# Optimization experiments

Hardware: AMD Instinct MI355X
Metric: run time of the kernel (lower is better)

The kernel has to match this reference:

```python
import jax, jax.numpy as jnp
import numpy as np

P = 0.8  # DropConnect keep probability
KERNELS = (3, 2)


def eps_contract(core, x, ks):
    """Contract one EPS core with all sliding ks x ks windows of x.
    core: (out, q**(ks*ks)); x: (b, h, w, q) -> (b, h-ks+1, w-ks+1, out).
    Builds the window tensor-product incrementally (small fixed ks*ks loop)."""
    b, h, w, q = x.shape
    H, W = h - ks + 1, w - ks + 1
    prod = None
    for di in range(ks):
        for dj in range(ks):
            pix = x[:, di:di + H, dj:dj + W, :]  # (b, H, W, q)
            if prod is None:
                prod = pix
            else:
                prod = (prod[..., :, None] * pix[..., None, :]).reshape(b, H, W, -1)
    # prod: (b, H, W, q**(ks*ks))
    return jnp.einsum('bhwk,ok->bhwo', prod, core)


def dropconnect_epses(epses):
    """Bernoulli(P) mask each core's components, rescale by 1/P (training mode)."""
    mkey = jax.random.key(42)
    out = []
    for i, core in enumerate(epses):
        mask = (jax.random.uniform(jax.random.fold_in(mkey, i), core.shape) < P).astype(core.dtype)
        out.append(mask * core / P)
    return out


def setup_inputs() -> dict:
    key = jax.random.key(0)
    k0, k1, k2, k3 = jax.random.split(key, 4)
    b = 128
    x = jax.random.uniform(k0, (b, 28, 28, 2), jnp.float32)  # quantum-encoded image
    d0 = 2 ** (3 * 3)   # 512 : first core input dim (q=2, ks=3)
    d1 = 6 ** (2 * 2)   # 1296: second core input dim (q=6, ks=2)
    eps0 = jax.random.normal(k1, (6, d0), jnp.float32) * d0 ** -0.5
    eps1 = jax.random.normal(k2, (10, d1), jnp.float32) * d1 ** -0.5
    in_features = 25 * 25 * 10  # (28 - (3+2) + 2)^2 * out_q
    W = jax.random.normal(k3, (10, in_features), jnp.float32) * (in_features ** -0.5 / 4.0)
    bias = jnp.zeros((10,), jnp.float32)
    return {"x": x, "eps0": eps0, "eps1": eps1, "W": W, "bias": bias}


def reference(x, eps0, eps1, W, bias):
    e0, e1 = dropconnect_epses((eps0, eps1))
    h = eps_contract(e0, x, KERNELS[0])   # (b, 26, 26, 6)
    h = eps_contract(e1, h, KERNELS[1])   # (b, 25, 25, 10)
    flat = h.reshape(h.shape[0], -1)      # b (h w q)
    return flat @ W.T + bias
```

## Files before the change

### kernel.cpp

```cpp
#include <hip/hip_runtime.h>
#include <hip/hip_bf16.h>
#include <stdint.h>

typedef __attribute__((ext_vector_type(8))) short short8;
typedef __attribute__((ext_vector_type(4))) float floatx4;
typedef __attribute__((ext_vector_type(4))) int intx4;

__device__ __forceinline__ void threefry2x32(uint32_t k0, uint32_t k1,
                                             uint32_t& x0, uint32_t& x1) {
  const uint32_t ks2 = k0 ^ k1 ^ 0x1BD11BDAu;
  uint32_t ks[3] = {k0, k1, ks2};
  const int rot[8] = {13, 15, 26, 6, 17, 29, 16, 24};
  x0 += ks[0];
  x1 += ks[1];
#pragma unroll
  for (int i = 0; i < 5; ++i) {
#pragma unroll
    for (int j = 0; j < 4; ++j) {
      const int r = rot[(i & 1) * 4 + j];
      x0 += x1;
      x1 = (x1 << r) | (x1 >> (32 - r));
      x1 ^= x0;
    }
    x0 += ks[(i + 1) % 3];
    x1 += ks[(i + 2) % 3] + (uint32_t)(i + 1);
  }
}

__device__ __forceinline__ float dropmask(int core, int e, float v) {
  uint32_t f0 = 0u, f1 = (uint32_t)core;
  threefry2x32(0u, 42u, f0, f1);
  uint32_t a = 0u, b = (uint32_t)e;
  threefry2x32(f0, f1, a, b);
  uint32_t bits = a ^ b;
  float u = __uint_as_float((bits >> 9) | 0x3F800000u) - 1.0f;
  float m = (u < 0.8f) ? 1.0f : 0.0f;
  return v * m / 0.8f;
}

__device__ __forceinline__ unsigned short f2bf(float f) {
  uint32_t u = __float_as_uint(f);
  uint32_t r = u + 0x7fffu + ((u >> 16) & 1u);
  return (unsigned short)(r >> 16);
}

union B2I { __hip_bfloat162 b; int i; };
__device__ __forceinline__ int pk_bf16(float lo, float hi) {
  B2I u;
  u.b = __float22bfloat162_rn(make_float2(lo, hi));
  return u.i;
}
union Frag { intx4 i; short8 s; };

__global__ void prep_kernel(const float* __restrict__ eps0,
                            const float* __restrict__ eps1,
                            unsigned short* __restrict__ bsw1,
                            unsigned short* __restrict__ bsw2,
                            float* __restrict__ out) {
  int idx = blockIdx.x * 256 + threadIdx.x;
  if (idx < 1280) out[idx] = 0.0f;
  if (idx < 8192) {
    int j = idx & 7, L = (idx >> 3) & 63, c = idx >> 9;
    int o = L & 15, q = L >> 4;
    int k = c * 32 + q * 8 + j;
    float v = 0.0f;
    if (o < 6) {
      int e = o * 512 + k;
      v = dropmask(0, e, eps0[e]);
    }
    bsw1[idx] = f2bf(v);
  } else {
    int t2 = idx - 8192;
    int j = t2 & 7, L = (t2 >> 3) & 63, c = t2 >> 9;
    int o = L & 15, q = L >> 4;
    int t = 45 * q + c;
    int m = t / 5, nk = 8 * (t % 5) + j;
    float v = 0.0f;
    if (o < 10 && nk < 36) {
      int e = o * 1296 + m * 36 + nk;
      v = dropmask(1, e, eps1[e]);
    }
    bsw2[t2] = f2bf(v);
  }
}

__device__ __forceinline__ float sel6(const float a[6], int k) {
  float r = a[0];
  r = (k == 1) ? a[1] : r;
  r = (k == 2) ? a[2] : r;
  r = (k == 3) ? a[3] : r;
  r = (k == 4) ? a[4] : r;
  r = (k == 5) ? a[5] : r;
  return r;
}

__global__ __launch_bounds__(256, 2) void stage1_mfma(
    const float* __restrict__ x, const unsigned short* __restrict__ bsw1,
    float* __restrict__ h) {
  __shared__ intx4 Bs[1024];
  {
    const intx4* src = (const intx4*)bsw1;
#pragma unroll
    for (int t = 0; t < 4; ++t)
      Bs[threadIdx.x + 256 * t] = src[threadIdx.x + 256 * t];
  }
  __syncthreads();

  const int lane = threadIdx.x & 63;
  const int wave = (blockIdx.x * 256 + threadIdx.x) >> 6;
  const int col = lane & 15, q = lane >> 4;
  const int pid = wave * 16 + col;
  const int b = pid / 676;
  const int rem = pid - b * 676;
  const int ii = rem / 26;
  const int jj = rem - ii * 26;

  const float2* x2 = (const float2*)x;
  float xv[9][2];
#pragma unroll
  for (int di = 0; di < 3; ++di)
#pragma unroll
    for (int dj = 0; dj < 3; ++dj) {
      float2 v = x2[(b * 28 + ii + di) * 28 + (jj + dj)];
      xv[di * 3 + dj][0] = v.x;
      xv[di * 3 + dj][1] = v.y;
    }

  float w3[8];
#pragma unroll
  for (int j = 0; j < 8; ++j)
    w3[j] = xv[6][(j >> 2) & 1] * xv[7][(j >> 1) & 1] * xv[8][j & 1];

  const float wq = xv[4][(q >> 1) & 1] * xv[5][q & 1];
  float t01[4], t23[4];
#pragma unroll
  for (int a = 0; a < 2; ++a)
#pragma unroll
    for (int d = 0; d < 2; ++d) {
      t01[a * 2 + d] = xv[0][a] * xv[1][d];
      t23[a * 2 + d] = xv[2][a] * xv[3][d] * wq;
    }

  floatx4 acc0 = {0.f, 0.f, 0.f, 0.f};
  floatx4 acc1 = {0.f, 0.f, 0.f, 0.f};
#pragma unroll
  for (int c = 0; c < 16; ++c) {
    Frag bf;
    bf.i = Bs[c * 64 + lane];
    const float w = t01[c >> 2] * t23[c & 3];
    float av[8];
#pragma unroll
    for (int j = 0; j < 8; ++j) av[j] = w * w3[j];
    Frag af;
    af.i.x = pk_bf16(av[0], av[1]);
    af.i.y = pk_bf16(av[2], av[3]);
    af.i.z = pk_bf16(av[4], av[5]);
    af.i.w = pk_bf16(av[6], av[7]);
    if (c & 1)
      acc1 = __builtin_amdgcn_mfma_f32_16x16x32_bf16(af.s, bf.s, acc1, 0, 0, 0);
    else
      acc0 = __builtin_amdgcn_mfma_f32_16x16x32_bf16(af.s, bf.s, acc0, 0, 0, 0);
  }
  const floatx4 acc = acc0 + acc1;
  if (col < 6) {
#pragma unroll
    for (int r = 0; r < 4; ++r) h[(wave * 16 + q * 4 + r) * 6 + col] = acc[r];
  }
}

__global__ __launch_bounds__(256, 2) void stage2_mfma(
    const float* __restrict__ h, const unsigned short* __restrict__ bsw2,
    float* __restrict__ flat) {
  __shared__ intx4 Bs[2880];
  {
    const intx4* src = (const intx4*)bsw2;
    for (int t = threadIdx.x; t < 2880; t += 256) Bs[t] = src[t];
  }
  __syncthreads();

  const int lane = threadIdx.x & 63;
  const int wave = (blockIdx.x * 256 + threadIdx.x) >> 6;
  const int col = lane & 15, q = lane >> 4;
  const int pid = wave * 16 + col;
  const int b = pid / 625;
  const int rem = pid - b * 625;
  const int ii = rem / 25;
  const int jj = rem - ii * 25;

  const float* hp = h + ((b * 26 + ii) * 26 + jj) * 6;
  float h00[6], h01[6], h10[6], h11[6];
  const float2* hp2a = (const float2*)(hp);
  const float2* hp2b = (const float2*)(hp + 156);
#pragma unroll
  for (int t = 0; t < 3; ++t) {
    float2 v0 = hp2a[t], v1 = hp2a[t + 3], v2 = hp2b[t], v3 = hp2b[t + 3];
    h00[2 * t] = v0.x; h00[2 * t + 1] = v0.y;
    h01[2 * t] = v1.x; h01[2 * t + 1] = v1.y;
    h10[2 * t] = v2.x; h10[2 * t + 1] = v2.y;
    h11[2 * t] = v3.x; h11[2 * t + 1] = v3.y;
  }

  floatx4 acc0 = {0.f, 0.f, 0.f, 0.f};
  floatx4 acc1 = {0.f, 0.f, 0.f, 0.f};
#pragma unroll
  for (int d = 0; d < 9; ++d) {
    const int m = 9 * q + d;
    const int ia = (m * 43) >> 8;
    const int ic = m - ia * 6;
    const float p01 = sel6(h00, ia) * sel6(h01, ic);
    float ph[6];
#pragma unroll
    for (int a = 0; a < 6; ++a) ph[a] = p01 * h10[a];
#pragma unroll
    for (int e = 0; e < 5; ++e) {
      Frag bf;
      bf.i = Bs[(d * 5 + e) * 64 + lane];
      const int n0 = 8 * e;
      float av[8];
#pragma unroll
      for (int j = 0; j < 8; ++j) {
        const int n = n0 + j;
        av[j] = (n < 36) ? ph[n / 6] * h11[n % 6] : 0.0f;
      }
      Frag af;
      af.i.x = pk_bf16(av[0], av[1]);
      af.i.y = pk_bf16(av[2], av[3]);
      af.i.z = pk_bf16(av[4], av[5]);
      af.i.w = pk_bf16(av[6], av[7]);
      if (e & 1)
        acc1 = __builtin_amdgcn_mfma_f32_16x16x32_bf16(af.s, bf.s, acc1, 0, 0, 0);
      else
        acc0 = __builtin_amdgcn_mfma_f32_16x16x32_bf16(af.s, bf.s, acc0, 0, 0, 0);
    }
  }
  const floatx4 acc = acc0 + acc1;
  if (col < 10) {
#pragma unroll
    for (int r = 0; r < 4; ++r)
      flat[(wave * 16 + q * 4 + r) * 10 + col] = acc[r];
  }
}

__global__ __launch_bounds__(256) void linear_kernel(
    const float* __restrict__ flat, const float* __restrict__ W,
    const float* __restrict__ bias, float* __restrict__ out) {
  const int b = blockIdx.x;
  const int c = blockIdx.y;
  const float* fb = flat + b * 6250 + c * 1250;
  const float* Wc = W + c * 1250;
  float acc[10];
#pragma unroll
  for (int o = 0; o < 10; ++o) acc[o] = 0.0f;
  for (int f = threadIdx.x; f < 1250; f += 256) {
    const float v = fb[f];
#pragma unroll
    for (int o = 0; o < 10; ++o) acc[o] += v * Wc[o * 6250 + f];
  }
#pragma unroll
  for (int o = 0; o < 10; ++o) {
#pragma unroll
    for (int s = 32; s > 0; s >>= 1) acc[o] += __shfl_xor(acc[o], s, 64);
  }
  __shared__ float red[4][10];
  const int lane = threadIdx.x & 63, wv = threadIdx.x >> 6;
  if (lane == 0) {
#pragma unroll
    for (int o = 0; o < 10; ++o) red[wv][o] = acc[o];
  }
  __syncthreads();
  if (threadIdx.x < 10) {
    const int o = threadIdx.x;
    float r = red[0][o] + red[1][o] + red[2][o] + red[3][o];
    if (c == 0) r += bias[o];
    atomicAdd(&out[b * 10 + o], r);
  }
}

extern "C" void kernel_launch(void* const* d_in, const int* in_sizes, int n_in,
                              void* d_out, int out_size, void* d_ws,
                              size_t ws_size, hipStream_t stream) {
  const float* x = (const float*)d_in[0];
  const float* eps0 = (const float*)d_in[1];
  const float* eps1 = (const float*)d_in[2];
  const float* W = (const float*)d_in[3];
  const float* bias = (const float*)d_in[4];
  float* out = (float*)d_out;

  char* wsb = (char*)d_ws;
  unsigned short* bsw1 = (unsigned short*)wsb;
  unsigned short* bsw2 = (unsigned short*)(wsb + 16384);
  float* h = (float*)(wsb + 65536);
  float* flat = (float*)(wsb + 65536 + 2076672);

  hipLaunchKernelGGL(prep_kernel, dim3(122), dim3(256), 0, stream, eps0, eps1,
                     bsw1, bsw2, out);
  hipLaunchKernelGGL(stage1_mfma, dim3(1352), dim3(256), 0, stream, x, bsw1,
                     h);
  hipLaunchKernelGGL(stage2_mfma, dim3(1250), dim3(256), 0, stream, h, bsw2,
                     flat);
  hipLaunchKernelGGL(linear_kernel, dim3(128, 5), dim3(256), 0, stream, flat,
                     W, bias, out);
}
```

Measured before the change: 105.1 us.

## Fuse both EPS stages and linear layer into one per-batch kernel

Merges stage1, stage2 and the linear layer into a single kernel with one 512-thread block per batch element. The intermediates h and flat stay in shared memory instead of global memory, and the B fragments are held in registers rather than LDS. The output is written directly, which removes the atomics and the zeroing in the prep kernel. The cost is that only 128 blocks run, which may underfill the GPU's CUs, and the 45 intx4 register fragments raise register pressure.

```diff
diff --git a/kernel.cpp b/kernel.cpp
--- a/kernel.cpp
+++ b/kernel.cpp
@@ -55,10 +55,8 @@
 __global__ void prep_kernel(const float* __restrict__ eps0,
                             const float* __restrict__ eps1,
                             unsigned short* __restrict__ bsw1,
-                            unsigned short* __restrict__ bsw2,
-                            float* __restrict__ out) {
+                            unsigned short* __restrict__ bsw2) {
   int idx = blockIdx.x * 256 + threadIdx.x;
-  if (idx < 1280) out[idx] = 0.0f;
   if (idx < 8192) {
     int j = idx & 7, L = (idx >> 3) & 63, c = idx >> 9;
     int o = L & 15, q = L >> 4;
@@ -94,185 +92,174 @@
   return r;
 }
 
-__global__ __launch_bounds__(256, 2) void stage1_mfma(
+__global__ __launch_bounds__(512, 2) void fused_kernel(
     const float* __restrict__ x, const unsigned short* __restrict__ bsw1,
-    float* __restrict__ h) {
-  __shared__ intx4 Bs[1024];
-  {
-    const intx4* src = (const intx4*)bsw1;
-#pragma unroll
-    for (int t = 0; t < 4; ++t)
-      Bs[threadIdx.x + 256 * t] = src[threadIdx.x + 256 * t];
-  }
-  __syncthreads();
-
-  const int lane = threadIdx.x & 63;
-  const int wave = (blockIdx.x * 256 + threadIdx.x) >> 6;
+    const unsigned short* __restrict__ bsw2, const float* __restrict__ W,
+    const float* __restrict__ bias, float* __restrict__ out) {
+  __shared__ float h_lds[4056];
+  __shared__ float flat_lds[6250];
+  __shared__ float red[8][10];
+
+  const int b = blockIdx.x;
+  const int tid = threadIdx.x;
+  const int lane = tid & 63;
+  const int wv = tid >> 6;
   const int col = lane & 15, q = lane >> 4;
-  const int pid = wave * 16 + col;
-  const int b = pid / 676;
-  const int rem = pid - b * 676;
-  const int ii = rem / 26;
-  const int jj = rem - ii * 26;
-
-  const float2* x2 = (const float2*)x;
-  float xv[9][2];
-#pragma unroll
-  for (int di = 0; di < 3; ++di)
-#pragma unroll
-    for (int dj = 0; dj < 3; ++dj) {
-      float2 v = x2[(b * 28 + ii + di) * 28 + (jj + dj)];
-      xv[di * 3 + dj][0] = v.x;
-      xv[di * 3 + dj][1] = v.y;
-    }
-
-  float w3[8];
-#pragma unroll
-  for (int j = 0; j < 8; ++j)
-    w3[j] = xv[6][(j >> 2) & 1] * xv[7][(j >> 1) & 1] * xv[8][j & 1];
-
-  const float wq = xv[4][(q >> 1) & 1] * xv[5][q & 1];
-  float t01[4], t23[4];
-#pragma unroll
-  for (int a = 0; a < 2; ++a)
-#pragma unroll
-    for (int d = 0; d < 2; ++d) {
-      t01[a * 2 + d] = xv[0][a] * xv[1][d];
-      t23[a * 2 + d] = xv[2][a] * xv[3][d] * wq;
-    }
-
-  floatx4 acc0 = {0.f, 0.f, 0.f, 0.f};
-  floatx4 acc1 = {0.f, 0.f, 0.f, 0.f};
-#pragma unroll
-  for (int c = 0; c < 16; ++c) {
-    Frag bf;
-    bf.i = Bs[c * 64 + lane];
-    const float w = t01[c >> 2] * t23[c & 3];
-    float av[8];
-#pragma unroll
-    for (int j = 0; j < 8; ++j) av[j] = w * w3[j];
-    Frag af;
-    af.i.x = pk_bf16(av[0], av[1]);
-    af.i.y = pk_bf16(av[2], av[3]);
-    af.i.z = pk_bf16(av[4], av[5]);
-    af.i.w = pk_bf16(av[6], av[7]);
-    if (c & 1)
-      acc1 = __builtin_amdgcn_mfma_f32_16x16x32_bf16(af.s, bf.s, acc1, 0, 0, 0);
-    else
-      acc0 = __builtin_amdgcn_mfma_f32_16x16x32_bf16(af.s, bf.s, acc0, 0, 0, 0);
-  }
-  const floatx4 acc = acc0 + acc1;
-  if (col < 6) {
-#pragma unroll
-    for (int r = 0; r < 4; ++r) h[(wave * 16 + q * 4 + r) * 6 + col] = acc[r];
-  }
-}
-
-__global__ __launch_bounds__(256, 2) void stage2_mfma(
-    const float* __restrict__ h, const unsigned short* __restrict__ bsw2,
-    float* __restrict__ flat) {
-  __shared__ intx4 Bs[2880];
-  {
-    const intx4* src = (const intx4*)bsw2;
-    for (int t = threadIdx.x; t < 2880; t += 256) Bs[t] = src[t];
-  }
-  __syncthreads();
-
-  const int lane = threadIdx.x & 63;
-  const int wave = (blockIdx.x * 256 + threadIdx.x) >> 6;
-  const int col = lane & 15, q = lane >> 4;
-  const int pid = wave * 16 + col;
-  const int b = pid / 625;
-  const int rem = pid - b * 625;
-  const int ii = rem / 25;
-  const int jj = rem - ii * 25;
-
-  const float* hp = h + ((b * 26 + ii) * 26 + jj) * 6;
-  float h00[6], h01[6], h10[6], h11[6];
-  const float2* hp2a = (const float2*)(hp);
-  const float2* hp2b = (const float2*)(hp + 156);
-#pragma unroll
-  for (int t = 0; t < 3; ++t) {
-    float2 v0 = hp2a[t], v1 = hp2a[t + 3], v2 = hp2b[t], v3 = hp2b[t + 3];
-    h00[2 * t] = v0.x; h00[2 * t + 1] = v0.y;
-    h01[2 * t] = v1.x; h01[2 * t + 1] = v1.y;
-    h10[2 * t] = v2.x; h10[2 * t + 1] = v2.y;
-    h11[2 * t] = v3.x; h11[2 * t + 1] = v3.y;
-  }
-
-  floatx4 acc0 = {0.f, 0.f, 0.f, 0.f};
-  floatx4 acc1 = {0.f, 0.f, 0.f, 0.f};
-#pragma unroll
-  for (int d = 0; d < 9; ++d) {
-    const int m = 9 * q + d;
-    const int ia = (m * 43) >> 8;
-    const int ic = m - ia * 6;
-    const float p01 = sel6(h00, ia) * sel6(h01, ic);
-    float ph[6];
-#pragma unroll
-    for (int a = 0; a < 6; ++a) ph[a] = p01 * h10[a];
-#pragma unroll
-    for (int e = 0; e < 5; ++e) {
+
+  intx4 bfr1[16];
+  const intx4* bsrc1 = (const intx4*)bsw1;
+#pragma unroll
+  for (int c = 0; c < 16; ++c) bfr1[c] = bsrc1[c * 64 + lane];
+
+  const float2* x2 = (const float2*)x + b * 784;
+#pragma unroll 1
+  for (int tile = wv; tile < 43; tile += 8) {
+    const int p_raw = tile * 16 + col;
+    const int p = p_raw < 676 ? p_raw : 675;
+    const int ii = p / 26, jj = p - (p / 26) * 26;
+
+    float xv[9][2];
+#pragma unroll
+    for (int di = 0; di < 3; ++di)
+#pragma unroll
+      for (int dj = 0; dj < 3; ++dj) {
+        float2 v = x2[(ii + di) * 28 + (jj + dj)];
+        xv[di * 3 + dj][0] = v.x;
+        xv[di * 3 + dj][1] = v.y;
+      }
+
+    float w3[8];
+#pragma unroll
+    for (int j = 0; j < 8; ++j)
+      w3[j] = xv[6][(j >> 2) & 1] * xv[7][(j >> 1) & 1] * xv[8][j & 1];
+
+    const float wq = xv[4][(q >> 1) & 1] * xv[5][q & 1];
+    float t01[4], t23[4];
+#pragma unroll
+    for (int a = 0; a < 2; ++a)
+#pragma unroll
+      for (int d = 0; d < 2; ++d) {
+        t01[a * 2 + d] = xv[0][a] * xv[1][d];
+        t23[a * 2 + d] = xv[2][a] * xv[3][d] * wq;
+      }
+
+    floatx4 acc0 = {0.f, 0.f, 0.f, 0.f};
+    floatx4 acc1 = {0.f, 0.f, 0.f, 0.f};
+#pragma unroll
+    for (int c = 0; c < 16; ++c) {
       Frag bf;
-      bf.i = Bs[(d * 5 + e) * 64 + lane];
-      const int n0 = 8 * e;
-      float av[8];
-#pragma unroll
-      for (int j = 0; j < 8; ++j) {
-        const int n = n0 + j;
-        av[j] = (n < 36) ? ph[n / 6] * h11[n % 6] : 0.0f;
-      }
+      bf.i = bfr1[c];
+      const float w = t01[c >> 2] * t23[c & 3];
       Frag af;
-      af.i.x = pk_bf16(av[0], av[1]);
-      af.i.y = pk_bf16(av[2], av[3]);
-      af.i.z = pk_bf16(av[4], av[5]);
-      af.i.w = pk_bf16(av[6], av[7]);
-      if (e & 1)
+      af.i.x = pk_bf16(w * w3[0], w * w3[1]);
+      af.i.y = pk_bf16(w * w3[2], w * w3[3]);
+      af.i.z = pk_bf16(w * w3[4], w * w3[5]);
+      af.i.w = pk_bf16(w * w3[6], w * w3[7]);
+      if (c & 1)
         acc1 = __builtin_amdgcn_mfma_f32_16x16x32_bf16(af.s, bf.s, acc1, 0, 0, 0);
       else
         acc0 = __builtin_amdgcn_mfma_f32_16x16x32_bf16(af.s, bf.s, acc0, 0, 0, 0);
     }
-  }
-  const floatx4 acc = acc0 + acc1;
-  if (col < 10) {
-#pragma unroll
-    for (int r = 0; r < 4; ++r)
-      flat[(wave * 16 + q * 4 + r) * 10 + col] = acc[r];
-  }
-}
-
-__global__ __launch_bounds__(256) void linear_kernel(
-    const float* __restrict__ flat, const float* __restrict__ W,
-    const float* __restrict__ bias, float* __restrict__ out) {
-  const int b = blockIdx.x;
-  const int c = blockIdx.y;
-  const float* fb = flat + b * 6250 + c * 1250;
-  const float* Wc = W + c * 1250;
+    const floatx4 acc = acc0 + acc1;
+    if (col < 6) {
+#pragma unroll
+      for (int r = 0; r < 4; ++r) {
+        const int pp = tile * 16 + q * 4 + r;
+        if (pp < 676) h_lds[pp * 6 + col] = acc[r];
+      }
+    }
+  }
+
+  intx4 bfr2[45];
+  const intx4* bsrc2 = (const intx4*)bsw2;
+#pragma unroll
+  for (int c = 0; c < 45; ++c) bfr2[c] = bsrc2[c * 64 + lane];
+
+  __syncthreads();
+
+#pragma unroll 1
+  for (int tile = wv; tile < 40; tile += 8) {
+    const int p_raw = tile * 16 + col;
+    const int p = p_raw < 625 ? p_raw : 624;
+    const int ii = p / 25, jj = p - (p / 25) * 25;
+    const int hbase = (ii * 26 + jj) * 6;
+
+    float h00[6], h01[6], h10[6], h11[6];
+#pragma unroll
+    for (int t = 0; t < 6; ++t) {
+      h00[t] = h_lds[hbase + t];
+      h01[t] = h_lds[hbase + 6 + t];
+      h10[t] = h_lds[hbase + 156 + t];
+      h11[t] = h_lds[hbase + 162 + t];
+    }
+
+    floatx4 acc0 = {0.f, 0.f, 0.f, 0.f};
+    floatx4 acc1 = {0.f, 0.f, 0.f, 0.f};
+#pragma unroll
+    for (int d = 0; d < 9; ++d) {
+      const int m = 9 * q + d;
+      const int ia = (m * 43) >> 8;
+      const int ic = m - ia * 6;
+      const float p01 = sel6(h00, ia) * sel6(h01, ic);
+      float ph[6];
+#pragma unroll
+      for (int a = 0; a < 6; ++a) ph[a] = p01 * h10[a];
+#pragma unroll
+      for (int e = 0; e < 5; ++e) {
+        Frag bf;
+        bf.i = bfr2[d * 5 + e];
+        const int n0 = 8 * e;
+        float av[8];
+#pragma unroll
+        for (int j = 0; j < 8; ++j) {
+          const int n = n0 + j;
+          av[j] = (n < 36) ? ph[n / 6] * h11[n % 6] : 0.0f;
+        }
+        Frag af;
+        af.i.x = pk_bf16(av[0], av[1]);
+        af.i.y = pk_bf16(av[2], av[3]);
+        af.i.z = pk_bf16(av[4], av[5]);
+        af.i.w = pk_bf16(av[6], av[7]);
+        if (e & 1)
+          acc1 = __builtin_amdgcn_mfma_f32_16x16x32_bf16(af.s, bf.s, acc1, 0, 0, 0);
+        else
+          acc0 = __builtin_amdgcn_mfma_f32_16x16x32_bf16(af.s, bf.s, acc0, 0, 0, 0);
+      }
+    }
+    const floatx4 acc = acc0 + acc1;
+    if (col < 10) {
+#pragma unroll
+      for (int r = 0; r < 4; ++r) {
+        const int pp = tile * 16 + q * 4 + r;
+        if (pp < 625) flat_lds[pp * 10 + col] = acc[r];
+      }
+    }
+  }
+  __syncthreads();
+
   float acc[10];
 #pragma unroll
   for (int o = 0; o < 10; ++o) acc[o] = 0.0f;
-  for (int f = threadIdx.x; f < 1250; f += 256) {
-    const float v = fb[f];
-#pragma unroll
-    for (int o = 0; o < 10; ++o) acc[o] += v * Wc[o * 6250 + f];
+  for (int f = tid; f < 6250; f += 512) {
+    const float v = flat_lds[f];
+#pragma unroll
+    for (int o = 0; o < 10; ++o) acc[o] += v * W[o * 6250 + f];
   }
 #pragma unroll
   for (int o = 0; o < 10; ++o) {
 #pragma unroll
     for (int s = 32; s > 0; s >>= 1) acc[o] += __shfl_xor(acc[o], s, 64);
   }
-  __shared__ float red[4][10];
-  const int lane = threadIdx.x & 63, wv = threadIdx.x >> 6;
   if (lane == 0) {
 #pragma unroll
     for (int o = 0; o < 10; ++o) red[wv][o] = acc[o];
   }
   __syncthreads();
-  if (threadIdx.x < 10) {
-    const int o = threadIdx.x;
-    float r = red[0][o] + red[1][o] + red[2][o] + red[3][o];
-    if (c == 0) r += bias[o];
-    atomicAdd(&out[b * 10 + o], r);
+  if (tid < 10) {
+    float r = bias[tid];
+#pragma unroll
+    for (int ww = 0; ww < 8; ++ww) r += red[ww][tid];
+    out[b * 10 + tid] = r;
   }
 }
 
@@ -289,15 +276,9 @@
   char* wsb = (char*)d_ws;
   unsigned short* bsw1 = (unsigned short*)wsb;
   unsigned short* bsw2 = (unsigned short*)(wsb + 16384);
-  float* h = (float*)(wsb + 65536);
-  float* flat = (float*)(wsb + 65536 + 2076672);
 
   hipLaunchKernelGGL(prep_kernel, dim3(122), dim3(256), 0, stream, eps0, eps1,
-                     bsw1, bsw2, out);
-  hipLaunchKernelGGL(stage1_mfma, dim3(1352), dim3(256), 0, stream, x, bsw1,
-                     h);
-  hipLaunchKernelGGL(stage2_mfma, dim3(1250), dim3(256), 0, stream, h, bsw2,
-                     flat);
-  hipLaunchKernelGGL(linear_kernel, dim3(128, 5), dim3(256), 0, stream, flat,
-                     W, bias, out);
-}
+                     bsw1, bsw2);
+  hipLaunchKernelGGL(fused_kernel, dim3(128), dim3(512), 0, stream, x, bsw1,
+                     bsw2, W, bias, out);
+}
```

Result: no change. 103.8 us (-1.2%).

## Switch MFMA stages to fp16 with packed half2 products and register-held B fragments

Applied to the files above, without the earlier changes.

Switches both contraction stages from bf16 to fp16 MFMA. The A-fragment outer products are now built with packed half2 multiplies instead of fp32 multiplies followed by bf16 packing. The shared-memory staging of the masked cores and its block barrier are replaced by per-lane global loads into registers, with an 8-deep prefetch ring in stage 2, and the launch-bounds occupancy hint rises from 2 to 4. Doing the products in half precision cuts conversion ALU work but changes rounding and narrows range, and the register-held fragments raise register pressure.

```diff
diff --git a/kernel.cpp b/kernel.cpp
--- a/kernel.cpp
+++ b/kernel.cpp
@@ -1,8 +1,8 @@
 #include <hip/hip_runtime.h>
-#include <hip/hip_bf16.h>
 #include <stdint.h>
 
-typedef __attribute__((ext_vector_type(8))) short short8;
+typedef _Float16 half8 __attribute__((ext_vector_type(8)));
+typedef _Float16 half2v __attribute__((ext_vector_type(2)));
 typedef __attribute__((ext_vector_type(4))) float floatx4;
 typedef __attribute__((ext_vector_type(4))) int intx4;
 
@@ -38,19 +38,14 @@
   return v * m / 0.8f;
 }
 
-__device__ __forceinline__ unsigned short f2bf(float f) {
-  uint32_t u = __float_as_uint(f);
-  uint32_t r = u + 0x7fffu + ((u >> 16) & 1u);
-  return (unsigned short)(r >> 16);
-}
-
-union B2I { __hip_bfloat162 b; int i; };
-__device__ __forceinline__ int pk_bf16(float lo, float hi) {
-  B2I u;
-  u.b = __float22bfloat162_rn(make_float2(lo, hi));
-  return u.i;
-}
-union Frag { intx4 i; short8 s; };
+union H2U { _Float16 h; unsigned short s; };
+__device__ __forceinline__ unsigned short f2h(float f) {
+  H2U u;
+  u.h = (_Float16)f;
+  return u.s;
+}
+
+union FragH { intx4 i; half8 h; half2v h2[4]; };
 
 __global__ void prep_kernel(const float* __restrict__ eps0,
                             const float* __restrict__ eps1,
@@ -68,7 +63,7 @@
       int e = o * 512 + k;
       v = dropmask(0, e, eps0[e]);
     }
-    bsw1[idx] = f2bf(v);
+    bsw1[idx] = f2h(v);
   } else {
     int t2 = idx - 8192;
     int j = t2 & 7, L = (t2 >> 3) & 63, c = t2 >> 9;
@@ -80,7 +75,7 @@
       int e = o * 1296 + m * 36 + nk;
       v = dropmask(1, e, eps1[e]);
     }
-    bsw2[t2] = f2bf(v);
+    bsw2[t2] = f2h(v);
   }
 }
 
@@ -94,21 +89,18 @@
   return r;
 }
 
-__global__ __launch_bounds__(256, 2) void stage1_mfma(
+__global__ __launch_bounds__(256, 4) void stage1_mfma(
     const float* __restrict__ x, const unsigned short* __restrict__ bsw1,
     float* __restrict__ h) {
-  __shared__ intx4 Bs[1024];
-  {
-    const intx4* src = (const intx4*)bsw1;
-#pragma unroll
-    for (int t = 0; t < 4; ++t)
-      Bs[threadIdx.x + 256 * t] = src[threadIdx.x + 256 * t];
-  }
-  __syncthreads();
-
   const int lane = threadIdx.x & 63;
   const int wave = (blockIdx.x * 256 + threadIdx.x) >> 6;
   const int col = lane & 15, q = lane >> 4;
+
+  intx4 bfr1[16];
+  const intx4* bsrc1 = (const intx4*)bsw1 + lane;
+#pragma unroll
+  for (int c = 0; c < 16; ++c) bfr1[c] = bsrc1[c * 64];
+
   const int pid = wave * 16 + col;
   const int b = pid / 676;
   const int rem = pid - b * 676;
@@ -126,10 +118,14 @@
       xv[di * 3 + dj][1] = v.y;
     }
 
-  float w3[8];
-#pragma unroll
-  for (int j = 0; j < 8; ++j)
-    w3[j] = xv[6][(j >> 2) & 1] * xv[7][(j >> 1) & 1] * xv[8][j & 1];
+  half2v w3p[4];
+#pragma unroll
+  for (int p2 = 0; p2 < 4; ++p2) {
+    const int j0 = 2 * p2, j1 = j0 + 1;
+    const float a0 = xv[6][(j0 >> 2) & 1] * xv[7][(j0 >> 1) & 1] * xv[8][j0 & 1];
+    const float a1 = xv[6][(j1 >> 2) & 1] * xv[7][(j1 >> 1) & 1] * xv[8][j1 & 1];
+    w3p[p2] = half2v{(_Float16)a0, (_Float16)a1};
+  }
 
   const float wq = xv[4][(q >> 1) & 1] * xv[5][q & 1];
   float t01[4], t23[4];
@@ -145,21 +141,19 @@
   floatx4 acc1 = {0.f, 0.f, 0.f, 0.f};
 #pragma unroll
   for (int c = 0; c < 16; ++c) {
-    Frag bf;
-    bf.i = Bs[c * 64 + lane];
-    const float w = t01[c >> 2] * t23[c & 3];
-    float av[8];
-#pragma unroll
-    for (int j = 0; j < 8; ++j) av[j] = w * w3[j];
-    Frag af;
-    af.i.x = pk_bf16(av[0], av[1]);
-    af.i.y = pk_bf16(av[2], av[3]);
-    af.i.z = pk_bf16(av[4], av[5]);
-    af.i.w = pk_bf16(av[6], av[7]);
+    FragH bf;
+    bf.i = bfr1[c];
+    const _Float16 wh = (_Float16)(t01[c >> 2] * t23[c & 3]);
+    const half2v w2 = {wh, wh};
+    FragH af;
+    af.h2[0] = w2 * w3p[0];
+    af.h2[1] = w2 * w3p[1];
+    af.h2[2] = w2 * w3p[2];
+    af.h2[3] = w2 * w3p[3];
     if (c & 1)
-      acc1 = __builtin_amdgcn_mfma_f32_16x16x32_bf16(af.s, bf.s, acc1, 0, 0, 0);
+      acc1 = __builtin_amdgcn_mfma_f32_16x16x32_f16(af.h, bf.h, acc1, 0, 0, 0);
     else
-      acc0 = __builtin_amdgcn_mfma_f32_16x16x32_bf16(af.s, bf.s, acc0, 0, 0, 0);
+      acc0 = __builtin_amdgcn_mfma_f32_16x16x32_f16(af.h, bf.h, acc0, 0, 0, 0);
   }
   const floatx4 acc = acc0 + acc1;
   if (col < 6) {
@@ -168,16 +162,9 @@
   }
 }
 
-__global__ __launch_bounds__(256, 2) void stage2_mfma(
+__global__ __launch_bounds__(256, 4) void stage2_mfma(
     const float* __restrict__ h, const unsigned short* __restrict__ bsw2,
     float* __restrict__ flat) {
-  __shared__ intx4 Bs[2880];
-  {
-    const intx4* src = (const intx4*)bsw2;
-    for (int t = threadIdx.x; t < 2880; t += 256) Bs[t] = src[t];
-  }
-  __syncthreads();
-
   const int lane = threadIdx.x & 63;
   const int wave = (blockIdx.x * 256 + threadIdx.x) >> 6;
   const int col = lane & 15, q = lane >> 4;
@@ -187,6 +174,11 @@
   const int ii = rem / 25;
   const int jj = rem - ii * 25;
 
+  const intx4* bsrc = (const intx4*)bsw2 + lane;
+  intx4 ring[8];
+#pragma unroll
+  for (int c = 0; c < 8; ++c) ring[c] = bsrc[c * 64];
+
   const float* hp = h + ((b * 26 + ii) * 26 + jj) * 6;
   float h00[6], h01[6], h10[6], h11[6];
   const float2* hp2a = (const float2*)(hp);
@@ -200,38 +192,45 @@
     h11[2 * t] = v3.x; h11[2 * t + 1] = v3.y;
   }
 
-  floatx4 acc0 = {0.f, 0.f, 0.f, 0.f};
-  floatx4 acc1 = {0.f, 0.f, 0.f, 0.f};
+  half2v p23p[20];
+#pragma unroll
+  for (int t = 0; t < 18; ++t) {
+    const int n0 = 2 * t, n1 = 2 * t + 1;
+    const float f0 = h10[n0 / 6] * h11[n0 % 6];
+    const float f1 = h10[n1 / 6] * h11[n1 % 6];
+    p23p[t] = half2v{(_Float16)f0, (_Float16)f1};
+  }
+  p23p[18] = half2v{(_Float16)0.f, (_Float16)0.f};
+  p23p[19] = half2v{(_Float16)0.f, (_Float16)0.f};
+
+  float P01s[9];
 #pragma unroll
   for (int d = 0; d < 9; ++d) {
     const int m = 9 * q + d;
     const int ia = (m * 43) >> 8;
     const int ic = m - ia * 6;
-    const float p01 = sel6(h00, ia) * sel6(h01, ic);
-    float ph[6];
-#pragma unroll
-    for (int a = 0; a < 6; ++a) ph[a] = p01 * h10[a];
-#pragma unroll
-    for (int e = 0; e < 5; ++e) {
-      Frag bf;
-      bf.i = Bs[(d * 5 + e) * 64 + lane];
-      const int n0 = 8 * e;
-      float av[8];
-#pragma unroll
-      for (int j = 0; j < 8; ++j) {
-        const int n = n0 + j;
-        av[j] = (n < 36) ? ph[n / 6] * h11[n % 6] : 0.0f;
-      }
-      Frag af;
-      af.i.x = pk_bf16(av[0], av[1]);
-      af.i.y = pk_bf16(av[2], av[3]);
-      af.i.z = pk_bf16(av[4], av[5]);
-      af.i.w = pk_bf16(av[6], av[7]);
-      if (e & 1)
-        acc1 = __builtin_amdgcn_mfma_f32_16x16x32_bf16(af.s, bf.s, acc1, 0, 0, 0);
-      else
-        acc0 = __builtin_amdgcn_mfma_f32_16x16x32_bf16(af.s, bf.s, acc0, 0, 0, 0);
-    }
+    P01s[d] = sel6(h00, ia) * sel6(h01, ic);
+  }
+
+  floatx4 acc0 = {0.f, 0.f, 0.f, 0.f};
+  floatx4 acc1 = {0.f, 0.f, 0.f, 0.f};
+#pragma unroll
+  for (int c = 0; c < 45; ++c) {
+    FragH bf;
+    bf.i = ring[c & 7];
+    if (c + 8 < 45) ring[c & 7] = bsrc[(c + 8) * 64];
+    const _Float16 ph = (_Float16)P01s[c / 5];
+    const half2v p2 = {ph, ph};
+    const int pb = 4 * (c % 5);
+    FragH af;
+    af.h2[0] = p2 * p23p[pb + 0];
+    af.h2[1] = p2 * p23p[pb + 1];
+    af.h2[2] = p2 * p23p[pb + 2];
+    af.h2[3] = p2 * p23p[pb + 3];
+    if (c & 1)
+      acc1 = __builtin_amdgcn_mfma_f32_16x16x32_f16(af.h, bf.h, acc1, 0, 0, 0);
+    else
+      acc0 = __builtin_amdgcn_mfma_f32_16x16x32_f16(af.h, bf.h, acc0, 0, 0, 0);
   }
   const floatx4 acc = acc0 + acc1;
   if (col < 10) {
```

New measurement: 110.3 us. 5.0% more time.
